# Kernel optimization log

Hardware: AMD Instinct MI355X
Metric: run time of the kernel (lower is better)

## Reference

```python
import jax, jax.numpy as jnp
import numpy as np

B, T = 64, 1024
ATTN_DIM, RNN_DIM, ENC_DIM = 128, 1024, 512
N_FILT, KSIZE = 32, 31
PAD = (KSIZE - 1) // 2


def setup_inputs() -> dict:
    key = jax.random.key(0)
    ks = jax.random.split(key, 11)
    query = jax.random.normal(ks[0], (B, RNN_DIM), dtype=jnp.float32)
    keys = jax.random.normal(ks[1], (B, T, ENC_DIM), dtype=jnp.float32)
    values = jax.random.normal(ks[2], (B, T, ENC_DIM), dtype=jnp.float32)
    attention_weights_cum = jax.random.uniform(ks[3], (B, T), dtype=jnp.float32)
    mask = jnp.zeros((B, T), dtype=bool)
    s = 0.02
    W_loc_conv = jax.random.normal(ks[4], (N_FILT, 1, KSIZE), dtype=jnp.float32) * s
    W_loc_proj = jax.random.normal(ks[5], (ATTN_DIM, N_FILT), dtype=jnp.float32) * s
    W_query = jax.random.normal(ks[6], (ATTN_DIM, RNN_DIM), dtype=jnp.float32) * s
    W_key = jax.random.normal(ks[7], (ATTN_DIM, ENC_DIM), dtype=jnp.float32) * s
    W_value = jax.random.normal(ks[8], (ENC_DIM, ENC_DIM), dtype=jnp.float32) * s
    W_attn = jax.random.normal(ks[9], (1, ATTN_DIM), dtype=jnp.float32) * s
    return {
        "query": query, "keys": keys, "values": values,
        "attention_weights_cum": attention_weights_cum, "mask": mask,
        "W_loc_conv": W_loc_conv, "W_loc_proj": W_loc_proj,
        "W_query": W_query, "W_key": W_key, "W_value": W_value, "W_attn": W_attn,
    }


def reference(query, keys, values, attention_weights_cum, mask,
              W_loc_conv, W_loc_proj, W_query, W_key, W_value, W_attn):
    # location features: conv1d over cumulative attention, (B,1,T) -> (B,N_FILT,T)
    loc = jax.lax.conv_general_dilated(
        attention_weights_cum[:, None, :], W_loc_conv,
        window_strides=(1,), padding=[(PAD, PAD)],
        dimension_numbers=("NCH", "OIH", "NCH"))
    # (B,T,N_FILT) @ W_loc_proj.T -> (B,T,ATTN_DIM)
    loc_feat = jnp.einsum("bft,af->bta", loc, W_loc_proj)
    q_proj = query @ W_query.T                      # (B, ATTN_DIM)
    k_proj = jnp.einsum("bte,ae->bta", keys, W_key)  # (B, T, ATTN_DIM)
    energies = jnp.tanh(q_proj[:, None, :] + k_proj + loc_feat)
    scores = jnp.einsum("bta,a->bt", energies, W_attn[0])  # (B, T)
    scores = jnp.where(mask, -jnp.inf, scores)
    attn = jax.nn.softmax(scores, axis=-1)
    v_proj = jnp.einsum("bte,fe->btf", values, W_value)  # (B, T, ENC_DIM)
    context = jnp.einsum("bt,btf->bf", attn, v_proj)      # (B, ENC_DIM)
    return context, attn
```

## Files before the change

### kernel.cpp

```cpp
#include <hip/hip_runtime.h>
#include <math.h>

#define B_   64
#define T_   1024
#define AD   128
#define RD   1024
#define ED   512
#define NF   32
#define KS   31
#define PADW 15

#define SA   72
#define SL   40

typedef short bf16x8 __attribute__((ext_vector_type(8)));
typedef float f32x4  __attribute__((ext_vector_type(4)));

__device__ __forceinline__ short f2bf(float x) {
  union { float f; unsigned u; } v; v.f = x;
  unsigned r = (v.u + 0x7FFFu + ((v.u >> 16) & 1u)) >> 16;
  return (short)r;
}

__device__ __forceinline__ float tanh_fast(float x) {
  float t = __expf(2.0f * x);
  return (t - 1.0f) * __builtin_amdgcn_rcpf(t + 1.0f);
}

__global__ __launch_bounds__(256) void prep_kernel(
    const float* __restrict__ Wk, const float* __restrict__ Wlp,
    const float* __restrict__ awc, const float* __restrict__ Wc,
    const float* __restrict__ query, const float* __restrict__ Wq,
    short* __restrict__ Wk16, short* __restrict__ Wlp16,
    short* __restrict__ loc_g, float* __restrict__ qp) {
  __shared__ float sh_awc[128 + KS - 1];
  __shared__ float sh_wc[NF * KS];
  __shared__ float sh_q[RD];
  __shared__ float sh_red[AD];
  const int blk = blockIdx.x, tid = threadIdx.x;

  if (blk < 68) {
    int p = blk * 256 + tid;
    const float* src; short* dst; int off;
    if (p < 16384) { src = Wk; dst = Wk16; off = p; }
    else           { src = Wlp; dst = Wlp16; off = p - 16384; }
    float4 v = *(const float4*)&src[off * 4];
    short4 h = { f2bf(v.x), f2bf(v.y), f2bf(v.z), f2bf(v.w) };
    *(short4*)&dst[off * 4] = h;
  } else if (blk < 580) {
    int cb = blk - 68;
    int b = cb >> 3, t0 = (cb & 7) * 128;
    for (int i = tid; i < NF * KS; i += 256) sh_wc[i] = Wc[i];
    if (tid < 128 + KS - 1) {
      int gt = t0 - PADW + tid;
      sh_awc[tid] = (gt >= 0 && gt < T_) ? awc[b * T_ + gt] : 0.0f;
    }
    __syncthreads();
    const int t = tid & 127, fh = (tid >> 7) * 16;
    for (int fq = 0; fq < 4; ++fq) {
      float s0 = 0.f, s1 = 0.f, s2 = 0.f, s3 = 0.f;
      const float* w0 = &sh_wc[(fh + fq * 4 + 0) * KS];
      const float* w1 = &sh_wc[(fh + fq * 4 + 1) * KS];
      const float* w2 = &sh_wc[(fh + fq * 4 + 2) * KS];
      const float* w3 = &sh_wc[(fh + fq * 4 + 3) * KS];
#pragma unroll
      for (int k = 0; k < KS; ++k) {
        float aw = sh_awc[t + k];
        s0 += w0[k] * aw; s1 += w1[k] * aw; s2 += w2[k] * aw; s3 += w3[k] * aw;
      }
      short4 h = { f2bf(s0), f2bf(s1), f2bf(s2), f2bf(s3) };
      *(short4*)&loc_g[((size_t)(b * T_ + t0 + t)) * NF + fh + fq * 4] = h;
    }
  } else {
    int b = blk - 580;
    *(float4*)&sh_q[tid * 4] = *(const float4*)&query[b * RD + tid * 4];
    __syncthreads();
    const int a = tid & 127, kh = tid >> 7;
    const float* wr = &Wq[(size_t)a * RD + kh * 512];
    const float* qr = &sh_q[kh * 512];
    float acc = 0.f;
    for (int e = 0; e < 512; e += 4) {
      float4 w = *(const float4*)&wr[e];
      acc += w.x * qr[e] + w.y * qr[e + 1] + w.z * qr[e + 2] + w.w * qr[e + 3];
    }
    if (kh == 1) sh_red[a] = acc;
    __syncthreads();
    if (kh == 0) qp[b * AD + a] = acc + sh_red[a];
  }
}

__global__ __launch_bounds__(256) void scores_kernel(
    const float* __restrict__ keys, const short* __restrict__ Wk16,
    const short* __restrict__ Wlp16, const short* __restrict__ loc_g,
    const float* __restrict__ qp, const float* __restrict__ Wa,
    float* __restrict__ scores) {
  __shared__ alignas(16) short As[64 * SA];
  __shared__ alignas(16) short Bs[128 * SA];
  __shared__ alignas(16) short Ls[64 * SL];
  __shared__ float qp_s[AD], wa_s[AD];
  __shared__ float sc_s[64 * 4];

  const int tid = threadIdx.x;
  const int b = blockIdx.y, t0 = blockIdx.x * 64;
  const int lane = tid & 63, wave = tid >> 6;
  const int m16 = lane & 15, s4 = lane >> 4;

  if (tid < AD) { qp_s[tid] = qp[b * AD + tid]; wa_s[tid] = Wa[tid]; }
  {
    int r = tid >> 2, c = tid & 3;
    *(int4*)&Ls[r * SL + c * 8] =
        *(const int4*)&loc_g[((size_t)(b * T_ + t0 + r)) * NF + c * 8];
  }

  f32x4 acc[4][2];
#pragma unroll
  for (int mt = 0; mt < 4; ++mt)
#pragma unroll
    for (int nt = 0; nt < 2; ++nt) acc[mt][nt] = (f32x4){0.f, 0.f, 0.f, 0.f};

  const float* kb = keys + ((size_t)(b * T_ + t0)) * ED;
  float4 pa[4]; int4 pb[4]; int4 pw[2];

#pragma unroll
  for (int i = 0; i < 4; ++i) {
    int p = i * 256 + tid;
    pa[i] = *(const float4*)&kb[(size_t)(p >> 4) * ED + (p & 15) * 4];
  }
#pragma unroll
  for (int i = 0; i < 4; ++i) {
    int p = i * 256 + tid;
    pb[i] = *(const int4*)&Wk16[(size_t)(p >> 3) * ED + (p & 7) * 8];
  }

  for (int kc = 0; kc < 8; ++kc) {
    __syncthreads();
#pragma unroll
    for (int i = 0; i < 4; ++i) {
      int p = i * 256 + tid, r = p >> 4, e4 = p & 15;
      short4 h = { f2bf(pa[i].x), f2bf(pa[i].y), f2bf(pa[i].z), f2bf(pa[i].w) };
      *(short4*)&As[r * SA + e4 * 4] = h;
    }
#pragma unroll
    for (int i = 0; i < 4; ++i) {
      int p = i * 256 + tid, r = p >> 3, c8 = p & 7;
      *(int4*)&Bs[r * SA + c8 * 8] = pb[i];
    }
    __syncthreads();
    if (kc < 7) {
      int ko = (kc + 1) * 64;
#pragma unroll
      for (int i = 0; i < 4; ++i) {
        int p = i * 256 + tid;
        pa[i] = *(const float4*)&kb[(size_t)(p >> 4) * ED + ko + (p & 15) * 4];
      }
#pragma unroll
      for (int i = 0; i < 4; ++i) {
        int p = i * 256 + tid;
        pb[i] = *(const int4*)&Wk16[(size_t)(p >> 3) * ED + ko + (p & 7) * 8];
      }
    } else {
#pragma unroll
      for (int i = 0; i < 2; ++i) {
        int p = i * 256 + tid;
        pw[i] = *(const int4*)&Wlp16[(p >> 2) * NF + (p & 3) * 8];
      }
    }
#pragma unroll
    for (int kk = 0; kk < 64; kk += 32) {
      const int ko = kk + s4 * 8;
      bf16x8 af[4], bfr[2];
#pragma unroll
      for (int mt = 0; mt < 4; ++mt)
        af[mt] = *(const bf16x8*)&As[(mt * 16 + m16) * SA + ko];
#pragma unroll
      for (int nt = 0; nt < 2; ++nt)
        bfr[nt] = *(const bf16x8*)&Bs[(wave * 32 + nt * 16 + m16) * SA + ko];
#pragma unroll
      for (int mt = 0; mt < 4; ++mt)
#pragma unroll
        for (int nt = 0; nt < 2; ++nt)
          acc[mt][nt] = __builtin_amdgcn_mfma_f32_16x16x32_bf16(
              af[mt], bfr[nt], acc[mt][nt], 0, 0, 0);
    }
  }

  __syncthreads();
#pragma unroll
  for (int i = 0; i < 2; ++i) {
    int p = i * 256 + tid;
    *(int4*)&Bs[(p >> 2) * SA + (p & 3) * 8] = pw[i];
  }
  __syncthreads();
  {
    const int ko = s4 * 8;
    bf16x8 af[4], bfr[2];
#pragma unroll
    for (int mt = 0; mt < 4; ++mt)
      af[mt] = *(const bf16x8*)&Ls[(mt * 16 + m16) * SL + ko];
#pragma unroll
    for (int nt = 0; nt < 2; ++nt)
      bfr[nt] = *(const bf16x8*)&Bs[(wave * 32 + nt * 16 + m16) * SA + ko];
#pragma unroll
    for (int mt = 0; mt < 4; ++mt)
#pragma unroll
      for (int nt = 0; nt < 2; ++nt)
        acc[mt][nt] = __builtin_amdgcn_mfma_f32_16x16x32_bf16(
            af[mt], bfr[nt], acc[mt][nt], 0, 0, 0);
  }

  float qv[2], wv[2];
#pragma unroll
  for (int nt = 0; nt < 2; ++nt) {
    int a = wave * 32 + nt * 16 + m16;
    qv[nt] = qp_s[a]; wv[nt] = wa_s[a];
  }
#pragma unroll
  for (int mt = 0; mt < 4; ++mt) {
#pragma unroll
    for (int r = 0; r < 4; ++r) {
      float p = wv[0] * tanh_fast(acc[mt][0][r] + qv[0]) +
                wv[1] * tanh_fast(acc[mt][1][r] + qv[1]);
      p += __shfl_xor(p, 1); p += __shfl_xor(p, 2);
      p += __shfl_xor(p, 4); p += __shfl_xor(p, 8);
      if (m16 == 0) sc_s[(mt * 16 + s4 * 4 + r) * 4 + wave] = p;
    }
  }
  __syncthreads();
  if (tid < 64) {
    float4 v = *(const float4*)&sc_s[tid * 4];
    scores[(size_t)b * T_ + t0 + tid] = v.x + v.y + v.z + v.w;
  }
}

__global__ __launch_bounds__(256) void softmax_kernel(
    const float* __restrict__ scores, const unsigned char* __restrict__ mask,
    float* __restrict__ attn) {
  const int b = blockIdx.x, tid = threadIdx.x;
  __shared__ float redm[4], reds[4];

  float4 s4 = *(const float4*)&scores[b * T_ + tid * 4];
  uchar4 m4 = *(const uchar4*)&mask[b * T_ + tid * 4];
  if (m4.x) s4.x = -INFINITY;
  if (m4.y) s4.y = -INFINITY;
  if (m4.z) s4.z = -INFINITY;
  if (m4.w) s4.w = -INFINITY;

  float mx = fmaxf(fmaxf(s4.x, s4.y), fmaxf(s4.z, s4.w));
#pragma unroll
  for (int off = 32; off >= 1; off >>= 1) mx = fmaxf(mx, __shfl_xor(mx, off, 64));
  if ((tid & 63) == 0) redm[tid >> 6] = mx;
  __syncthreads();
  mx = fmaxf(fmaxf(redm[0], redm[1]), fmaxf(redm[2], redm[3]));

  float e0 = expf(s4.x - mx), e1 = expf(s4.y - mx);
  float e2 = expf(s4.z - mx), e3 = expf(s4.w - mx);
  float sum = e0 + e1 + e2 + e3;
#pragma unroll
  for (int off = 32; off >= 1; off >>= 1) sum += __shfl_xor(sum, off, 64);
  if ((tid & 63) == 0) reds[tid >> 6] = sum;
  __syncthreads();
  sum = reds[0] + reds[1] + reds[2] + reds[3];

  float inv = 1.0f / sum;
  float4 o4 = { e0 * inv, e1 * inv, e2 * inv, e3 * inv };
  *(float4*)&attn[b * T_ + tid * 4] = o4;
}

__global__ __launch_bounds__(256) void wvsum_kernel(
    const float* __restrict__ values, const float* __restrict__ attn,
    float* __restrict__ wvp) {
  const int tc = blockIdx.x, b = blockIdx.y, tid = threadIdx.x;
  __shared__ float at_s[64];
  if (tid < 64) at_s[tid] = attn[b * T_ + tc * 64 + tid];
  __syncthreads();
  const int e4 = tid & 127, th = tid >> 7;
  const float* vb =
      values + ((size_t)(b * T_ + tc * 64 + th * 32)) * ED + e4 * 4;
  float4 acc = {0.f, 0.f, 0.f, 0.f};
#pragma unroll 8
  for (int t = 0; t < 32; ++t) {
    float a = at_s[th * 32 + t];
    float4 v = *(const float4*)&vb[(size_t)t * ED];
    acc.x = fmaf(a, v.x, acc.x); acc.y = fmaf(a, v.y, acc.y);
    acc.z = fmaf(a, v.z, acc.z); acc.w = fmaf(a, v.w, acc.w);
  }
  *(float4*)&wvp[((size_t)(b * 32 + tc * 2 + th)) * ED + e4 * 4] = acc;
}

__global__ __launch_bounds__(256) void context_kernel(
    const float* __restrict__ wvp, const float* __restrict__ Wv,
    float* __restrict__ ctx) {
  const int fq = blockIdx.x, b = blockIdx.y, tid = threadIdx.x;
  __shared__ float wv_s[ED];
  __shared__ float red[128];
  for (int e = tid; e < ED; e += 256) {
    float s = 0.f;
    const float* base = &wvp[(size_t)b * 32 * ED + e];
#pragma unroll
    for (int p = 0; p < 32; ++p) s += base[p * ED];
    wv_s[e] = s;
  }
  __syncthreads();
  const int fl = tid & 127, eh = tid >> 7;
  const int f = fq * 128 + fl;
  const float* wr = &Wv[(size_t)f * ED + eh * 256];
  const float* qr = &wv_s[eh * 256];
  float acc = 0.f;
  for (int e = 0; e < 256; e += 4) {
    float4 w = *(const float4*)&wr[e];
    acc += w.x * qr[e] + w.y * qr[e + 1] + w.z * qr[e + 2] + w.w * qr[e + 3];
  }
  if (eh == 1) red[fl] = acc;
  __syncthreads();
  if (eh == 0) ctx[b * ED + f] = acc + red[fl];
}

extern "C" void kernel_launch(void* const* d_in, const int* in_sizes, int n_in,
                              void* d_out, int out_size, void* d_ws, size_t ws_size,
                              hipStream_t stream) {
  const float* query = (const float*)d_in[0];
  const float* keys  = (const float*)d_in[1];
  const float* values= (const float*)d_in[2];
  const float* awc   = (const float*)d_in[3];
  const unsigned char* mask = (const unsigned char*)d_in[4];
  const float* Wc    = (const float*)d_in[5];
  const float* Wlp   = (const float*)d_in[6];
  const float* Wq    = (const float*)d_in[7];
  const float* Wk    = (const float*)d_in[8];
  const float* Wv    = (const float*)d_in[9];
  const float* Wa    = (const float*)d_in[10];

  float* ctx  = (float*)d_out;
  float* attn = (float*)d_out + B_ * ED;

  float* ws = (float*)d_ws;
  float* qp      = ws;
  float* scoresB = qp + B_ * AD;
  float* wvp     = scoresB + B_ * T_;
  short* Wk16    = (short*)(wvp + (size_t)B_ * 32 * ED);
  short* Wlp16   = Wk16 + AD * ED;
  short* loc_g   = Wlp16 + AD * NF;

  prep_kernel<<<644, 256, 0, stream>>>(Wk, Wlp, awc, Wc, query, Wq,
                                       Wk16, Wlp16, loc_g, qp);
  scores_kernel<<<dim3(16, B_), 256, 0, stream>>>(keys, Wk16, Wlp16, loc_g,
                                                  qp, Wa, scoresB);
  softmax_kernel<<<B_, 256, 0, stream>>>(scoresB, mask, attn);
  wvsum_kernel<<<dim3(16, B_), 256, 0, stream>>>(values, attn, wvp);
  context_kernel<<<dim3(4, B_), 256, 0, stream>>>(wvp, Wv, ctx);
}
```

Measured before the change: 360.4 us.

## Pre-convert keys to bf16 and load GEMM tiles via global_load_lds with swizzle

Adds a pass in the prep kernel that converts the full keys tensor to bf16 in workspace. The scores kernel then streams bf16 tiles straight into LDS with global_load_lds using an XOR-swizzled layout, replacing the register prefetch and in-kernel conversion. Tiles grow to 128x128 per block with a 2x2 wave arrangement, and the location projection GEMM runs first. The cost is an extra full read of fp32 keys plus a bf16 write and re-read, and the main loop no longer overlaps its loads with compute.

```diff
diff --git a/kernel.cpp b/kernel.cpp
--- a/kernel.cpp
+++ b/kernel.cpp
@@ -10,11 +10,17 @@
 #define KS   31
 #define PADW 15
 
-#define SA   72
-#define SL   40
-
 typedef short bf16x8 __attribute__((ext_vector_type(8)));
 typedef float f32x4  __attribute__((ext_vector_type(4)));
+
+typedef __attribute__((address_space(1))) unsigned gu32;
+typedef __attribute__((address_space(3))) unsigned lu32;
+
+__device__ __forceinline__ void gll16(const void* g, void* l) {
+  __builtin_amdgcn_global_load_lds(
+      (gu32*)(unsigned long long)g,
+      (lu32*)(unsigned)(unsigned long long)l, 16, 0, 0);
+}
 
 __device__ __forceinline__ short f2bf(float x) {
   union { float f; unsigned u; } v; v.f = x;
@@ -27,10 +33,12 @@
   return (t - 1.0f) * __builtin_amdgcn_rcpf(t + 1.0f);
 }
 
+#define KB_  2048
 __global__ __launch_bounds__(256) void prep_kernel(
-    const float* __restrict__ Wk, const float* __restrict__ Wlp,
-    const float* __restrict__ awc, const float* __restrict__ Wc,
-    const float* __restrict__ query, const float* __restrict__ Wq,
+    const float* __restrict__ keys, const float* __restrict__ Wk,
+    const float* __restrict__ Wlp, const float* __restrict__ awc,
+    const float* __restrict__ Wc, const float* __restrict__ query,
+    const float* __restrict__ Wq, short* __restrict__ keys16,
     short* __restrict__ Wk16, short* __restrict__ Wlp16,
     short* __restrict__ loc_g, float* __restrict__ qp) {
   __shared__ float sh_awc[128 + KS - 1];
@@ -39,16 +47,25 @@
   __shared__ float sh_red[AD];
   const int blk = blockIdx.x, tid = threadIdx.x;
 
-  if (blk < 68) {
-    int p = blk * 256 + tid;
+  if (blk < KB_) {
+    size_t base = (size_t)blk * 4096 + tid;
+#pragma unroll
+    for (int i = 0; i < 16; ++i) {
+      size_t p = base + (size_t)i * 256;
+      float4 v = *(const float4*)&keys[p * 4];
+      short4 h = { f2bf(v.x), f2bf(v.y), f2bf(v.z), f2bf(v.w) };
+      *(short4*)&keys16[p * 4] = h;
+    }
+  } else if (blk < KB_ + 68) {
+    int p = (blk - KB_) * 256 + tid;
     const float* src; short* dst; int off;
     if (p < 16384) { src = Wk; dst = Wk16; off = p; }
     else           { src = Wlp; dst = Wlp16; off = p - 16384; }
     float4 v = *(const float4*)&src[off * 4];
     short4 h = { f2bf(v.x), f2bf(v.y), f2bf(v.z), f2bf(v.w) };
     *(short4*)&dst[off * 4] = h;
-  } else if (blk < 580) {
-    int cb = blk - 68;
+  } else if (blk < KB_ + 68 + 512) {
+    int cb = blk - (KB_ + 68);
     int b = cb >> 3, t0 = (cb & 7) * 128;
     for (int i = tid; i < NF * KS; i += 256) sh_wc[i] = Wc[i];
     if (tid < 128 + KS - 1) {
@@ -72,7 +89,7 @@
       *(short4*)&loc_g[((size_t)(b * T_ + t0 + t)) * NF + fh + fq * 4] = h;
     }
   } else {
-    int b = blk - 580;
+    int b = blk - (KB_ + 68 + 512);
     *(float4*)&sh_q[tid * 4] = *(const float4*)&query[b * RD + tid * 4];
     __syncthreads();
     const int a = tid & 127, kh = tid >> 7;
@@ -89,147 +106,110 @@
   }
 }
 
-__global__ __launch_bounds__(256) void scores_kernel(
-    const float* __restrict__ keys, const short* __restrict__ Wk16,
+__global__ __launch_bounds__(256, 2) void scores_kernel(
+    const short* __restrict__ keys16, const short* __restrict__ Wk16,
     const short* __restrict__ Wlp16, const short* __restrict__ loc_g,
     const float* __restrict__ qp, const float* __restrict__ Wa,
     float* __restrict__ scores) {
-  __shared__ alignas(16) short As[64 * SA];
-  __shared__ alignas(16) short Bs[128 * SA];
-  __shared__ alignas(16) short Ls[64 * SL];
+  __shared__ alignas(16) short As[128 * 64];
+  __shared__ alignas(16) short Bs[128 * 64];
   __shared__ float qp_s[AD], wa_s[AD];
-  __shared__ float sc_s[64 * 4];
+  __shared__ float sc_s[128 * 2];
 
   const int tid = threadIdx.x;
-  const int b = blockIdx.y, t0 = blockIdx.x * 64;
+  const int b = blockIdx.y, t0 = blockIdx.x * 128;
   const int lane = tid & 63, wave = tid >> 6;
+  const int wm = wave >> 1, wn = wave & 1;
   const int m16 = lane & 15, s4 = lane >> 4;
 
   if (tid < AD) { qp_s[tid] = qp[b * AD + tid]; wa_s[tid] = Wa[tid]; }
+
   {
-    int r = tid >> 2, c = tid & 3;
-    *(int4*)&Ls[r * SL + c * 8] =
-        *(const int4*)&loc_g[((size_t)(b * T_ + t0 + r)) * NF + c * 8];
-  }
-
-  f32x4 acc[4][2];
-#pragma unroll
-  for (int mt = 0; mt < 4; ++mt)
-#pragma unroll
-    for (int nt = 0; nt < 2; ++nt) acc[mt][nt] = (f32x4){0.f, 0.f, 0.f, 0.f};
-
-  const float* kb = keys + ((size_t)(b * T_ + t0)) * ED;
-  float4 pa[4]; int4 pb[4]; int4 pw[2];
-
-#pragma unroll
-  for (int i = 0; i < 4; ++i) {
-    int p = i * 256 + tid;
-    pa[i] = *(const float4*)&kb[(size_t)(p >> 4) * ED + (p & 15) * 4];
-  }
-#pragma unroll
-  for (int i = 0; i < 4; ++i) {
-    int p = i * 256 + tid;
-    pb[i] = *(const int4*)&Wk16[(size_t)(p >> 3) * ED + (p & 7) * 8];
-  }
+    const int r = lane >> 2, cb = lane & 3;
+#pragma unroll
+    for (int i = 0; i < 2; ++i) {
+      int row = wave * 32 + i * 16;
+      gll16(&loc_g[((size_t)(b * T_ + t0 + row + r)) * NF + cb * 8],
+            &As[row * 32]);
+      gll16(&Wlp16[(row + r) * NF + cb * 8], &Bs[row * 32]);
+    }
+  }
+  __syncthreads();
+
+  f32x4 acc[4][4];
+  {
+    bf16x8 af[4], bfr[4];
+#pragma unroll
+    for (int mt = 0; mt < 4; ++mt)
+      af[mt] = *(const bf16x8*)&As[(wm * 64 + mt * 16 + m16) * 32 + s4 * 8];
+#pragma unroll
+    for (int nt = 0; nt < 4; ++nt)
+      bfr[nt] = *(const bf16x8*)&Bs[(wn * 64 + nt * 16 + m16) * 32 + s4 * 8];
+#pragma unroll
+    for (int mt = 0; mt < 4; ++mt)
+#pragma unroll
+      for (int nt = 0; nt < 4; ++nt)
+        acc[mt][nt] = __builtin_amdgcn_mfma_f32_16x16x32_bf16(
+            af[mt], bfr[nt], (f32x4){0.f, 0.f, 0.f, 0.f}, 0, 0, 0);
+  }
+
+  const int r8 = lane >> 3, cb8 = lane & 7;
+  const int cbg = cb8 ^ r8;
+  const size_t kb = ((size_t)(b * T_ + t0)) * ED;
 
   for (int kc = 0; kc < 8; ++kc) {
     __syncthreads();
 #pragma unroll
     for (int i = 0; i < 4; ++i) {
-      int p = i * 256 + tid, r = p >> 4, e4 = p & 15;
-      short4 h = { f2bf(pa[i].x), f2bf(pa[i].y), f2bf(pa[i].z), f2bf(pa[i].w) };
-      *(short4*)&As[r * SA + e4 * 4] = h;
-    }
-#pragma unroll
-    for (int i = 0; i < 4; ++i) {
-      int p = i * 256 + tid, r = p >> 3, c8 = p & 7;
-      *(int4*)&Bs[r * SA + c8 * 8] = pb[i];
-    }
-    __syncthreads();
-    if (kc < 7) {
-      int ko = (kc + 1) * 64;
-#pragma unroll
-      for (int i = 0; i < 4; ++i) {
-        int p = i * 256 + tid;
-        pa[i] = *(const float4*)&kb[(size_t)(p >> 4) * ED + ko + (p & 15) * 4];
-      }
-#pragma unroll
-      for (int i = 0; i < 4; ++i) {
-        int p = i * 256 + tid;
-        pb[i] = *(const int4*)&Wk16[(size_t)(p >> 3) * ED + ko + (p & 7) * 8];
-      }
-    } else {
-#pragma unroll
-      for (int i = 0; i < 2; ++i) {
-        int p = i * 256 + tid;
-        pw[i] = *(const int4*)&Wlp16[(p >> 2) * NF + (p & 3) * 8];
-      }
-    }
-#pragma unroll
-    for (int kk = 0; kk < 64; kk += 32) {
-      const int ko = kk + s4 * 8;
-      bf16x8 af[4], bfr[2];
+      int row = wave * 32 + i * 8;
+      gll16(&keys16[kb + (size_t)(row + r8) * ED + kc * 64 + cbg * 8],
+            &As[row * 64]);
+      gll16(&Wk16[(size_t)(row + r8) * ED + kc * 64 + cbg * 8],
+            &Bs[row * 64]);
+    }
+    __syncthreads();
+#pragma unroll
+    for (int kk2 = 0; kk2 < 2; ++kk2) {
+      const int j = kk2 * 4 + s4;
+      const int ca = (j ^ (m16 & 7)) * 8;
+      bf16x8 af[4], bfr[4];
 #pragma unroll
       for (int mt = 0; mt < 4; ++mt)
-        af[mt] = *(const bf16x8*)&As[(mt * 16 + m16) * SA + ko];
-#pragma unroll
-      for (int nt = 0; nt < 2; ++nt)
-        bfr[nt] = *(const bf16x8*)&Bs[(wave * 32 + nt * 16 + m16) * SA + ko];
+        af[mt] = *(const bf16x8*)&As[(wm * 64 + mt * 16 + m16) * 64 + ca];
+#pragma unroll
+      for (int nt = 0; nt < 4; ++nt)
+        bfr[nt] = *(const bf16x8*)&Bs[(wn * 64 + nt * 16 + m16) * 64 + ca];
 #pragma unroll
       for (int mt = 0; mt < 4; ++mt)
 #pragma unroll
-        for (int nt = 0; nt < 2; ++nt)
+        for (int nt = 0; nt < 4; ++nt)
           acc[mt][nt] = __builtin_amdgcn_mfma_f32_16x16x32_bf16(
               af[mt], bfr[nt], acc[mt][nt], 0, 0, 0);
     }
   }
 
-  __syncthreads();
-#pragma unroll
-  for (int i = 0; i < 2; ++i) {
-    int p = i * 256 + tid;
-    *(int4*)&Bs[(p >> 2) * SA + (p & 3) * 8] = pw[i];
-  }
-  __syncthreads();
-  {
-    const int ko = s4 * 8;
-    bf16x8 af[4], bfr[2];
-#pragma unroll
-    for (int mt = 0; mt < 4; ++mt)
-      af[mt] = *(const bf16x8*)&Ls[(mt * 16 + m16) * SL + ko];
-#pragma unroll
-    for (int nt = 0; nt < 2; ++nt)
-      bfr[nt] = *(const bf16x8*)&Bs[(wave * 32 + nt * 16 + m16) * SA + ko];
-#pragma unroll
-    for (int mt = 0; mt < 4; ++mt)
-#pragma unroll
-      for (int nt = 0; nt < 2; ++nt)
-        acc[mt][nt] = __builtin_amdgcn_mfma_f32_16x16x32_bf16(
-            af[mt], bfr[nt], acc[mt][nt], 0, 0, 0);
-  }
-
-  float qv[2], wv[2];
-#pragma unroll
-  for (int nt = 0; nt < 2; ++nt) {
-    int a = wave * 32 + nt * 16 + m16;
+  float qv[4], wv[4];
+#pragma unroll
+  for (int nt = 0; nt < 4; ++nt) {
+    int a = wn * 64 + nt * 16 + m16;
     qv[nt] = qp_s[a]; wv[nt] = wa_s[a];
   }
 #pragma unroll
   for (int mt = 0; mt < 4; ++mt) {
 #pragma unroll
     for (int r = 0; r < 4; ++r) {
-      float p = wv[0] * tanh_fast(acc[mt][0][r] + qv[0]) +
-                wv[1] * tanh_fast(acc[mt][1][r] + qv[1]);
+      float p = 0.f;
+#pragma unroll
+      for (int nt = 0; nt < 4; ++nt)
+        p += wv[nt] * tanh_fast(acc[mt][nt][r] + qv[nt]);
       p += __shfl_xor(p, 1); p += __shfl_xor(p, 2);
       p += __shfl_xor(p, 4); p += __shfl_xor(p, 8);
-      if (m16 == 0) sc_s[(mt * 16 + s4 * 4 + r) * 4 + wave] = p;
-    }
-  }
-  __syncthreads();
-  if (tid < 64) {
-    float4 v = *(const float4*)&sc_s[tid * 4];
-    scores[(size_t)b * T_ + t0 + tid] = v.x + v.y + v.z + v.w;
-  }
+      if (m16 == 0) sc_s[(wm * 64 + mt * 16 + s4 * 4 + r) * 2 + wn] = p;
+    }
+  }
+  __syncthreads();
+  if (tid < 128)
+    scores[(size_t)b * T_ + t0 + tid] = sc_s[tid * 2] + sc_s[tid * 2 + 1];
 }
 
 __global__ __launch_bounds__(256) void softmax_kernel(
@@ -340,11 +320,12 @@
   short* Wk16    = (short*)(wvp + (size_t)B_ * 32 * ED);
   short* Wlp16   = Wk16 + AD * ED;
   short* loc_g   = Wlp16 + AD * NF;
-
-  prep_kernel<<<644, 256, 0, stream>>>(Wk, Wlp, awc, Wc, query, Wq,
-                                       Wk16, Wlp16, loc_g, qp);
-  scores_kernel<<<dim3(16, B_), 256, 0, stream>>>(keys, Wk16, Wlp16, loc_g,
-                                                  qp, Wa, scoresB);
+  short* keys16  = loc_g + (size_t)B_ * T_ * NF;
+
+  prep_kernel<<<KB_ + 68 + 512 + 64, 256, 0, stream>>>(
+      keys, Wk, Wlp, awc, Wc, query, Wq, keys16, Wk16, Wlp16, loc_g, qp);
+  scores_kernel<<<dim3(8, B_), 256, 0, stream>>>(keys16, Wk16, Wlp16, loc_g,
+                                                 qp, Wa, scoresB);
   softmax_kernel<<<B_, 256, 0, stream>>>(scoresB, mask, attn);
   wvsum_kernel<<<dim3(16, B_), 256, 0, stream>>>(values, attn, wvp);
   context_kernel<<<dim3(4, B_), 256, 0, stream>>>(wvp, Wv, ctx);
```

Result: faster. 347.9 us (-3.5%).
